# Kernel tuning notes

Hardware: AMD Instinct MI355X
Metric: run time of the kernel (lower is better)

Reference implementation:

```python
import jax, jax.numpy as jnp
import numpy as np

HIDDEN = 1024
INTER = 4096
N_EXPERTS = 8
TOP_K = 2
INIT_STD = 0.02


def setup_inputs() -> dict:
    key = jax.random.key(0)
    ks = jax.random.split(key, 6)
    x = jax.random.normal(ks[0], (2, 1024, HIDDEN), dtype=jnp.float32)
    Wg = jax.random.normal(ks[1], (N_EXPERTS, HIDDEN), dtype=jnp.float32) * INIT_STD
    # Expert MLP params, stacked over experts. W1: [E, H, I], W2: [E, I, H].
    W1 = jax.random.normal(ks[2], (N_EXPERTS, HIDDEN, INTER), dtype=jnp.float32) * INIT_STD
    b1 = jnp.zeros((N_EXPERTS, INTER), dtype=jnp.float32)
    W2 = jax.random.normal(ks[3], (N_EXPERTS, INTER, HIDDEN), dtype=jnp.float32) * INIT_STD
    b2 = jnp.zeros((N_EXPERTS, HIDDEN), dtype=jnp.float32)
    return {"x": x, "Wg": Wg, "W1": W1, "b1": b1, "W2": W2, "b2": b2}


def reference(x, Wg, W1, b1, W2, b2):
    orig_shape = x.shape
    xt = x.reshape(-1, HIDDEN)              # [T, H]
    T = xt.shape[0]

    # Gating: top-k logits -> softmax over the k selected experts.
    logits = xt @ Wg.T                      # [T, E]
    topk_logits, topk_idx = jax.lax.top_k(logits, TOP_K)   # [T, K]
    w = jax.nn.softmax(topk_logits, axis=-1)               # [T, K]

    # Scatter top-k weights into a dense [T, E] gate matrix (zeros elsewhere).
    rows = jnp.arange(T)[:, None]
    gates = jnp.zeros((T, N_EXPERTS), xt.dtype).at[rows, topk_idx].add(w)

    # Dense expert compute (mathematically identical: non-selected experts get
    # gate weight 0). Expert MLP: Linear -> GELU (exact, erf) -> Linear.
    h = jnp.einsum('th,ehi->tei', xt, W1) + b1             # [T, E, I]
    h = jax.nn.gelu(h, approximate=False)
    o = jnp.einsum('tei,eih->teh', h, W2) + b2             # [T, E, H]
    y = jnp.einsum('te,teh->th', gates, o)                 # [T, H]
    return y.reshape(orig_shape)
```

## Files before the change

### kernel.cpp

```cpp
#include <hip/hip_runtime.h>
#include <hip/hip_bf16.h>

#define HID 1024
#define INTER 4096
#define NE 8
#define NTOK 2048
#define MAXROWS 5120

typedef __attribute__((ext_vector_type(8))) short short8v;
typedef __attribute__((ext_vector_type(4))) float f32x4;

__device__ __forceinline__ unsigned short f2bf(float f) {
  unsigned int u = __builtin_bit_cast(unsigned int, f);
  u = (u + 0x7FFFu + ((u >> 16) & 1u)) >> 16;
  return (unsigned short)u;
}

typedef const __attribute__((address_space(1))) unsigned int* gas_t;
typedef __attribute__((address_space(3))) unsigned int* las_t;
__device__ __forceinline__ void gld16(const unsigned short* g, unsigned short* l) {
  __builtin_amdgcn_global_load_lds((gas_t)(const void*)g, (las_t)(void*)l, 16, 0, 0);
}

__global__ __launch_bounds__(256) void convx_kernel(const float* __restrict__ in,
                                                    unsigned short* __restrict__ out) {
  size_t i = (size_t)blockIdx.x * 256 + threadIdx.x;
  f32x4 v = *(const f32x4*)&in[i * 4];
  uint2 r;
  r.x = (unsigned int)f2bf(v[0]) | ((unsigned int)f2bf(v[1]) << 16);
  r.y = (unsigned int)f2bf(v[2]) | ((unsigned int)f2bf(v[3]) << 16);
  *(uint2*)&out[i * 4] = r;
}

__global__ __launch_bounds__(256) void tconv_kernel(const float* __restrict__ in,
                                                    unsigned short* __restrict__ out,
                                                    int R, int C) {
  __shared__ float t[64][65];
  const int z = blockIdx.z;
  const int r0 = blockIdx.y * 64, c0 = blockIdx.x * 64;
  const int tr = threadIdx.x / 16;
  const int tc = (threadIdx.x % 16) * 4;
  const float* ip = in + ((size_t)z * R + r0) * (size_t)C + c0;
#pragma unroll
  for (int p = 0; p < 4; ++p) {
    f32x4 v = *(const f32x4*)&ip[(size_t)(p * 16 + tr) * C + tc];
    t[p * 16 + tr][tc + 0] = v[0];
    t[p * 16 + tr][tc + 1] = v[1];
    t[p * 16 + tr][tc + 2] = v[2];
    t[p * 16 + tr][tc + 3] = v[3];
  }
  __syncthreads();
  unsigned short* op = out + ((size_t)z * C + c0) * (size_t)R + r0;
#pragma unroll
  for (int p = 0; p < 4; ++p) {
    int c = p * 16 + tr;
    unsigned int a0 = (unsigned int)f2bf(t[tc + 0][c]) | ((unsigned int)f2bf(t[tc + 1][c]) << 16);
    unsigned int a1 = (unsigned int)f2bf(t[tc + 2][c]) | ((unsigned int)f2bf(t[tc + 3][c]) << 16);
    uint2 val; val.x = a0; val.y = a1;
    *(uint2*)&op[(size_t)c * R + tc] = val;
  }
}

__global__ __launch_bounds__(256) void gating_kernel(const float* __restrict__ x,
                                                     const float* __restrict__ wg,
                                                     int* __restrict__ tok_e,
                                                     float* __restrict__ tok_w) {
  const int t = blockIdx.x;
  float acc[NE];
#pragma unroll
  for (int e = 0; e < NE; ++e) acc[e] = 0.f;
  for (int k = threadIdx.x; k < HID; k += 256) {
    float xv = x[(size_t)t * HID + k];
#pragma unroll
    for (int e = 0; e < NE; ++e) acc[e] += xv * wg[e * HID + k];
  }
#pragma unroll
  for (int e = 0; e < NE; ++e) {
#pragma unroll
    for (int off = 32; off >= 1; off >>= 1) acc[e] += __shfl_xor(acc[e], off, 64);
  }
  __shared__ float red[4][NE];
  const int wave = threadIdx.x >> 6, lane = threadIdx.x & 63;
  if (lane == 0) {
#pragma unroll
    for (int e = 0; e < NE; ++e) red[wave][e] = acc[e];
  }
  __syncthreads();
  if (threadIdx.x == 0) {
    float l[NE];
#pragma unroll
    for (int e = 0; e < NE; ++e) l[e] = red[0][e] + red[1][e] + red[2][e] + red[3][e];
    int i0 = 0;
#pragma unroll
    for (int e = 1; e < NE; ++e) if (l[e] > l[i0]) i0 = e;
    int i1 = -1;
#pragma unroll
    for (int e = 0; e < NE; ++e) {
      if (e == i0) continue;
      if (i1 < 0 || l[e] > l[i1]) i1 = e;
    }
    float e1 = __expf(l[i1] - l[i0]);
    float w0 = 1.f / (1.f + e1);
    tok_e[t * 2 + 0] = i0;
    tok_e[t * 2 + 1] = i1;
    tok_w[t * 2 + 0] = w0;
    tok_w[t * 2 + 1] = 1.f - w0;
  }
}

__global__ __launch_bounds__(512) void routing_kernel(const int* __restrict__ tok_e,
                                                      int* __restrict__ list_tok,
                                                      int* __restrict__ tok_gslot,
                                                      int* __restrict__ offs_out) {
  __shared__ int cnts[NE];
  __shared__ int offs_s[NE + 1];
  const int e = threadIdx.x >> 6, lane = threadIdx.x & 63;
  int c = 0;
  for (int base = 0; base < NTOK; base += 64) {
    int tok = base + lane;
    int e0 = tok_e[tok * 2], e1 = tok_e[tok * 2 + 1];
    bool m = (e0 == e) || (e1 == e);
    unsigned long long mask = __ballot(m);
    c += __popcll(mask);
  }
  if (lane == 0) cnts[e] = c;
  __syncthreads();
  if (threadIdx.x == 0) {
    int o = 0;
    for (int i = 0; i < NE; ++i) { offs_s[i] = o; o += (cnts[i] + 127) & ~127; }
    offs_s[NE] = o;
    for (int i = 0; i <= NE; ++i) offs_out[i] = offs_s[i];
  }
  __syncthreads();
  const int off = offs_s[e];
  int run = 0;
  for (int base = 0; base < NTOK; base += 64) {
    int tok = base + lane;
    int e0 = tok_e[tok * 2], e1 = tok_e[tok * 2 + 1];
    bool m = (e0 == e) || (e1 == e);
    unsigned long long mask = __ballot(m);
    int pos = run + __popcll(mask & ((1ull << lane) - 1ull));
    if (m) {
      int gs = off + pos;
      list_tok[gs] = tok;
      tok_gslot[tok * 2 + ((e0 == e) ? 0 : 1)] = gs;
    }
    run += __popcll(mask);
  }
  const int cnt = cnts[e];
  const int padded = (cnt + 127) & ~127;
  for (int p = cnt + lane; p < padded; p += 64) list_tok[off + p] = 0;
}

template <int KTOT, int NTOT, bool FIRST, int NSPLIT>
__global__ __launch_bounds__(256, 2) void moe_gemm(const unsigned short* __restrict__ Abase,
                                                   const unsigned short* __restrict__ Bbase,
                                                   const float* __restrict__ bias,
                                                   const int* __restrict__ list_tok,
                                                   const int* __restrict__ offs,
                                                   void* __restrict__ outp) {
  constexpr int KS = KTOT / NSPLIT;
  constexpr int NT = KS / 64;
  constexpr int nM = MAXROWS / 128;
  constexpr int nN = NTOT / 128;
  __shared__ __align__(16) unsigned short lds[2][2][8192];

  const int nwg = nN * nM * NSPLIT;
  int wg = blockIdx.x;
  wg = (wg & 7) * (nwg >> 3) + (wg >> 3);
  const int ks = (NSPLIT > 1) ? (wg / (nM * nN)) : 0;
  const int rem = wg % (nM * nN);
  const int mt = rem % nM;
  const int nt = rem / nM;
  const int grow0 = mt * 128;
  if (grow0 >= offs[NE]) return;
  int e = 0;
#pragma unroll
  for (int i = 1; i < NE; ++i) if (grow0 >= offs[i]) e = i;
  const int n0 = nt * 128;
  const int k0 = ks * KS;

  const int tid = threadIdx.x;
  const int wave = tid >> 6, lane = tid & 63;

  const int scol = ((lane & 7) * 8) ^ ((lane >> 3) * 8);
  const unsigned short* ag[4];
  const unsigned short* bg[4];
#pragma unroll
  for (int i = 0; i < 4; ++i) {
    const int row = i * 32 + wave * 8 + (lane >> 3);
    size_t arow;
    if (FIRST) arow = (size_t)list_tok[grow0 + row] * KTOT;
    else       arow = (size_t)(grow0 + row) * KTOT;
    ag[i] = Abase + arow + k0 + scol;
    bg[i] = Bbase + (size_t)e * NTOT * KTOT + (size_t)(n0 + row) * KTOT + k0 + scol;
  }

  const int wm = wave >> 1, wn = wave & 1;
  const int fr = lane & 15;
  const int kq = (lane >> 4) * 8;
  const int swz = (fr & 7) * 8;
  int aoff[4], boff[4];
#pragma unroll
  for (int m = 0; m < 4; ++m) aoff[m] = (wm * 64 + m * 16 + fr) * 64;
#pragma unroll
  for (int n = 0; n < 4; ++n) boff[n] = (wn * 64 + n * 16 + fr) * 64;
  const int kc0 = (kq) ^ swz;
  const int kc1 = (32 + kq) ^ swz;

  f32x4 acc[4][4] = {};

#pragma unroll
  for (int i = 0; i < 4; ++i) gld16(ag[i], &lds[0][0][i * 2048 + wave * 512]);
#pragma unroll
  for (int i = 0; i < 4; ++i) gld16(bg[i], &lds[0][1][i * 2048 + wave * 512]);
  __syncthreads();

  for (int t = 0; t < NT; ++t) {
    if (t + 1 < NT) {
      const int bb = (t + 1) & 1;
#pragma unroll
      for (int i = 0; i < 4; ++i) gld16(ag[i] + (t + 1) * 64, &lds[bb][0][i * 2048 + wave * 512]);
#pragma unroll
      for (int i = 0; i < 4; ++i) gld16(bg[i] + (t + 1) * 64, &lds[bb][1][i * 2048 + wave * 512]);
    }
    const unsigned short* A = &lds[t & 1][0][0];
    const unsigned short* B = &lds[t & 1][1][0];
#pragma unroll
    for (int kk = 0; kk < 2; ++kk) {
      const int kc = kk ? kc1 : kc0;
      short8v af[4], bf[4];
#pragma unroll
      for (int m = 0; m < 4; ++m) af[m] = *(const short8v*)&A[aoff[m] + kc];
#pragma unroll
      for (int n = 0; n < 4; ++n) bf[n] = *(const short8v*)&B[boff[n] + kc];
#pragma unroll
      for (int m = 0; m < 4; ++m)
#pragma unroll
        for (int n = 0; n < 4; ++n)
          acc[m][n] = __builtin_amdgcn_mfma_f32_16x16x32_bf16(af[m], bf[n], acc[m][n], 0, 0, 0);
    }
    __syncthreads();
  }

  const int r4 = lane >> 4;
#pragma unroll
  for (int m = 0; m < 4; ++m) {
#pragma unroll
    for (int n = 0; n < 4; ++n) {
      const int gcol = n0 + wn * 64 + n * 16 + fr;
      float bv = 0.f;
      if (FIRST) bv = bias[e * NTOT + gcol];
#pragma unroll
      for (int r = 0; r < 4; ++r) {
        const int grow = grow0 + wm * 64 + m * 16 + r4 * 4 + r;
        float v = acc[m][n][r] + bv;
        if (FIRST) {
          v = 0.5f * v * (1.0f + erff(v * 0.70710678118654752f));
          ((unsigned short*)outp)[(size_t)grow * NTOT + gcol] = f2bf(v);
        } else {
          ((float*)outp)[((size_t)ks * MAXROWS + grow) * NTOT + gcol] = v;
        }
      }
    }
  }
}

__global__ __launch_bounds__(256) void combine_kernel(const float* __restrict__ part,
                                                      const int* __restrict__ tok_gslot,
                                                      const int* __restrict__ tok_e,
                                                      const float* __restrict__ tok_w,
                                                      const float* __restrict__ b2,
                                                      float* __restrict__ y) {
  const int t = blockIdx.x;
  const int c = threadIdx.x * 4;
  const int gs0 = tok_gslot[t * 2 + 0], gs1 = tok_gslot[t * 2 + 1];
  const int e0 = tok_e[t * 2 + 0], e1 = tok_e[t * 2 + 1];
  const float w0 = tok_w[t * 2 + 0], w1 = tok_w[t * 2 + 1];
  const size_t P1 = (size_t)MAXROWS * HID;
  f32x4 a0 = *(const f32x4*)&part[(size_t)gs0 * HID + c];
  f32x4 a1 = *(const f32x4*)&part[P1 + (size_t)gs0 * HID + c];
  f32x4 d0 = *(const f32x4*)&part[(size_t)gs1 * HID + c];
  f32x4 d1 = *(const f32x4*)&part[P1 + (size_t)gs1 * HID + c];
  f32x4 bb0 = *(const f32x4*)&b2[e0 * HID + c];
  f32x4 bb1 = *(const f32x4*)&b2[e1 * HID + c];
  f32x4 r;
#pragma unroll
  for (int i = 0; i < 4; ++i)
    r[i] = w0 * (a0[i] + a1[i] + bb0[i]) + w1 * (d0[i] + d1[i] + bb1[i]);
  *(f32x4*)&y[(size_t)t * HID + c] = r;
}

extern "C" void kernel_launch(void* const* d_in, const int* in_sizes, int n_in,
                              void* d_out, int out_size, void* d_ws, size_t ws_size,
                              hipStream_t stream) {
  const float* x  = (const float*)d_in[0];
  const float* wg = (const float*)d_in[1];
  const float* W1 = (const float*)d_in[2];
  const float* b1 = (const float*)d_in[3];
  const float* W2 = (const float*)d_in[4];
  const float* b2 = (const float*)d_in[5];
  float* y = (float*)d_out;

  unsigned char* ws = (unsigned char*)d_ws;
  size_t off = 0;
  unsigned short* w1t = (unsigned short*)(ws + off);
  float* part         = (float*)(ws + off);          off += (size_t)NE * HID * INTER * 2;
  unsigned short* w2t = (unsigned short*)(ws + off); off += (size_t)NE * INTER * HID * 2;
  unsigned short* xb  = (unsigned short*)(ws + off); off += (size_t)NTOK * HID * 2;
  unsigned short* h   = (unsigned short*)(ws + off); off += (size_t)MAXROWS * INTER * 2;
  int* tok_e          = (int*)(ws + off);            off += NTOK * 2 * 4;
  float* tok_w        = (float*)(ws + off);          off += NTOK * 2 * 4;
  int* tok_gslot      = (int*)(ws + off);            off += NTOK * 2 * 4;
  int* list_tok       = (int*)(ws + off);            off += MAXROWS * 4;
  int* offs           = (int*)(ws + off);            off += 64;
  (void)ws_size; (void)in_sizes; (void)n_in; (void)out_size;

  convx_kernel<<<(NTOK * HID / 4 + 255) / 256, 256, 0, stream>>>(x, xb);
  tconv_kernel<<<dim3(INTER / 64, HID / 64, NE), 256, 0, stream>>>(W1, w1t, HID, INTER);
  tconv_kernel<<<dim3(HID / 64, INTER / 64, NE), 256, 0, stream>>>(W2, w2t, INTER, HID);
  gating_kernel<<<NTOK, 256, 0, stream>>>(x, wg, tok_e, tok_w);
  routing_kernel<<<1, 512, 0, stream>>>(tok_e, list_tok, tok_gslot, offs);
  moe_gemm<HID, INTER, true, 1><<<(INTER / 128) * (MAXROWS / 128), 256, 0, stream>>>(
      xb, w1t, b1, list_tok, offs, (void*)h);
  moe_gemm<INTER, HID, false, 2><<<(HID / 128) * (MAXROWS / 128) * 2, 256, 0, stream>>>(
      h, w2t, b2, list_tok, offs, (void*)part);
  combine_kernel<<<NTOK, 256, 0, stream>>>(part, tok_gslot, tok_e, tok_w, b2, y);
}
```

Baseline: 250.9 us.

## Switch MoE GEMM to triple-buffered K=32 stages with single-barrier pipeline

```diff
diff --git a/kernel.cpp b/kernel.cpp
--- a/kernel.cpp
+++ b/kernel.cpp
@@ -153,17 +153,17 @@
 }
 
 template <int KTOT, int NTOT, bool FIRST, int NSPLIT>
-__global__ __launch_bounds__(256, 2) void moe_gemm(const unsigned short* __restrict__ Abase,
+__global__ __launch_bounds__(256, 3) void moe_gemm(const unsigned short* __restrict__ Abase,
                                                    const unsigned short* __restrict__ Bbase,
                                                    const float* __restrict__ bias,
                                                    const int* __restrict__ list_tok,
                                                    const int* __restrict__ offs,
                                                    void* __restrict__ outp) {
   constexpr int KS = KTOT / NSPLIT;
-  constexpr int NT = KS / 64;
+  constexpr int NT = KS / 32;
   constexpr int nM = MAXROWS / 128;
   constexpr int nN = NTOT / 128;
-  __shared__ __align__(16) unsigned short lds[2][2][8192];
+  __shared__ __align__(16) unsigned short lds[3][2][4096];
 
   const int nwg = nN * nM * NSPLIT;
   int wg = blockIdx.x;
@@ -183,65 +183,78 @@
   const int tid = threadIdx.x;
   const int wave = tid >> 6, lane = tid & 63;
 
-  const int scol = ((lane & 7) * 8) ^ ((lane >> 3) * 8);
-  const unsigned short* ag[4];
-  const unsigned short* bg[4];
-#pragma unroll
-  for (int i = 0; i < 4; ++i) {
-    const int row = i * 32 + wave * 8 + (lane >> 3);
+  const int srow = tid >> 2;
+  const int skc = (tid & 3) * 8;
+  const unsigned short* ag[2];
+  const unsigned short* bg[2];
+#pragma unroll
+  for (int j = 0; j < 2; ++j) {
+    const int row = srow + j * 64;
     size_t arow;
     if (FIRST) arow = (size_t)list_tok[grow0 + row] * KTOT;
     else       arow = (size_t)(grow0 + row) * KTOT;
-    ag[i] = Abase + arow + k0 + scol;
-    bg[i] = Bbase + (size_t)e * NTOT * KTOT + (size_t)(n0 + row) * KTOT + k0 + scol;
-  }
+    ag[j] = Abase + arow + k0 + skc;
+    bg[j] = Bbase + (size_t)e * NTOT * KTOT + (size_t)(n0 + row) * KTOT + k0 + skc;
+  }
+  const int wbase = wave * 512;
 
   const int wm = wave >> 1, wn = wave & 1;
   const int fr = lane & 15;
   const int kq = (lane >> 4) * 8;
-  const int swz = (fr & 7) * 8;
   int aoff[4], boff[4];
 #pragma unroll
-  for (int m = 0; m < 4; ++m) aoff[m] = (wm * 64 + m * 16 + fr) * 64;
-#pragma unroll
-  for (int n = 0; n < 4; ++n) boff[n] = (wn * 64 + n * 16 + fr) * 64;
-  const int kc0 = (kq) ^ swz;
-  const int kc1 = (32 + kq) ^ swz;
+  for (int m = 0; m < 4; ++m) aoff[m] = (wm * 64 + m * 16 + fr) * 32 + kq;
+#pragma unroll
+  for (int n = 0; n < 4; ++n) boff[n] = (wn * 64 + n * 16 + fr) * 32 + kq;
 
   f32x4 acc[4][4] = {};
 
-#pragma unroll
-  for (int i = 0; i < 4; ++i) gld16(ag[i], &lds[0][0][i * 2048 + wave * 512]);
-#pragma unroll
-  for (int i = 0; i < 4; ++i) gld16(bg[i], &lds[0][1][i * 2048 + wave * 512]);
-  __syncthreads();
-
-  for (int t = 0; t < NT; ++t) {
-    if (t + 1 < NT) {
-      const int bb = (t + 1) & 1;
-#pragma unroll
-      for (int i = 0; i < 4; ++i) gld16(ag[i] + (t + 1) * 64, &lds[bb][0][i * 2048 + wave * 512]);
-#pragma unroll
-      for (int i = 0; i < 4; ++i) gld16(bg[i] + (t + 1) * 64, &lds[bb][1][i * 2048 + wave * 512]);
-    }
-    const unsigned short* A = &lds[t & 1][0][0];
-    const unsigned short* B = &lds[t & 1][1][0];
-#pragma unroll
-    for (int kk = 0; kk < 2; ++kk) {
-      const int kc = kk ? kc1 : kc0;
-      short8v af[4], bf[4];
-#pragma unroll
-      for (int m = 0; m < 4; ++m) af[m] = *(const short8v*)&A[aoff[m] + kc];
-#pragma unroll
-      for (int n = 0; n < 4; ++n) bf[n] = *(const short8v*)&B[boff[n] + kc];
-#pragma unroll
-      for (int m = 0; m < 4; ++m)
-#pragma unroll
-        for (int n = 0; n < 4; ++n)
-          acc[m][n] = __builtin_amdgcn_mfma_f32_16x16x32_bf16(af[m], bf[n], acc[m][n], 0, 0, 0);
-    }
-    __syncthreads();
-  }
+#define STAGE(S, SLOT)                                             \
+  {                                                                \
+    gld16(ag[0] + (S) * 32, &lds[SLOT][0][wbase]);                 \
+    gld16(ag[1] + (S) * 32, &lds[SLOT][0][wbase + 2048]);          \
+    gld16(bg[0] + (S) * 32, &lds[SLOT][1][wbase]);                 \
+    gld16(bg[1] + (S) * 32, &lds[SLOT][1][wbase + 2048]);          \
+  }
+
+#define KITER(S, SL, DO_STAGE, VMSTR)                              \
+  {                                                                \
+    asm volatile("s_waitcnt vmcnt(" VMSTR ")" ::: "memory");       \
+    asm volatile("s_barrier" ::: "memory");                        \
+    const unsigned short* A = &lds[SL][0][0];                      \
+    const unsigned short* B = &lds[SL][1][0];                      \
+    short8v af[4];                                                 \
+    _Pragma("unroll")                                              \
+    for (int m = 0; m < 4; ++m) af[m] = *(const short8v*)&A[aoff[m]]; \
+    if (DO_STAGE) {                                                \
+      int s2 = (SL) + 2; if (s2 >= 3) s2 -= 3;                     \
+      STAGE((S) + 2, s2);                                          \
+    }                                                              \
+    __builtin_amdgcn_s_setprio(1);                                 \
+    _Pragma("unroll")                                              \
+    for (int n = 0; n < 4; ++n) {                                  \
+      short8v bf = *(const short8v*)&B[boff[n]];                   \
+      _Pragma("unroll")                                            \
+      for (int m = 0; m < 4; ++m)                                  \
+        acc[m][n] = __builtin_amdgcn_mfma_f32_16x16x32_bf16(af[m], bf, acc[m][n], 0, 0, 0); \
+    }                                                              \
+    __builtin_amdgcn_s_setprio(0);                                 \
+  }
+
+  STAGE(0, 0);
+  STAGE(1, 1);
+
+  int sl = 0;
+  for (int s = 0; s < NT - 2; ++s) {
+    KITER(s, sl, true, "4");
+    sl = sl + 1; if (sl >= 3) sl = 0;
+  }
+  KITER(NT - 2, sl, false, "4");
+  sl = sl + 1; if (sl >= 3) sl = 0;
+  KITER(NT - 1, sl, false, "0");
+
+#undef KITER
+#undef STAGE
 
   const int r4 = lane >> 4;
 #pragma unroll
```

Result: no change. 251.4 us (+0.2%).
